# Optimization experiments

Measured on AMD Instinct MI355X. Metric: run time of the kernel, lower is better.

The kernel has to match this reference:

```python
import jax, jax.numpy as jnp
import numpy as np

TOP_K = 2
NUM_EXPERTS = 8
NORM_TOPK_PROB = True


def setup_inputs() -> dict:
    key = jax.random.key(0)
    k0, k1, k2, k3, k4 = jax.random.split(key, 5)
    B, S, H, I, E = 2, 512, 1024, 768, NUM_EXPERTS
    scale = 0.02
    return {
        "hidden_states": jax.random.normal(k0, (B, S, H), dtype=jnp.float32),
        "gate_w": jax.random.normal(k1, (H, E), dtype=jnp.float32) * scale,
        "w_gate": jax.random.normal(k2, (E, H, I), dtype=jnp.float32) * scale,
        "w_up": jax.random.normal(k3, (E, H, I), dtype=jnp.float32) * scale,
        "w_down": jax.random.normal(k4, (E, I, H), dtype=jnp.float32) * scale,
    }


def reference(hidden_states, gate_w, w_gate, w_up, w_down):
    orig_shape = hidden_states.shape
    H = orig_shape[-1]
    x = hidden_states.reshape(-1, H)  # [T, H]
    E = gate_w.shape[-1]

    # Router: softmax in float32, then top-k and optional renormalization.
    router_logits = x @ gate_w  # [T, E]
    routing_probs = jax.nn.softmax(router_logits.astype(jnp.float32), axis=-1)
    routing_weights, selected_experts = jax.lax.top_k(routing_probs, TOP_K)  # [T, K]
    if NORM_TOPK_PROB:
        routing_weights = routing_weights / routing_weights.sum(axis=-1, keepdims=True)
    routing_weights = routing_weights.astype(x.dtype)

    # Combine weights per (token, expert): sum over top-k slots (handles duplicates
    # exactly like the original index_add over per-slot contributions).
    cw = (jax.nn.one_hot(selected_experts, E, dtype=x.dtype)
          * routing_weights[..., None]).sum(axis=1)  # [T, E]

    # Dense per-expert MLP; zero combine weight => zero contribution, matching the
    # gather-MLP-scatter loop's math.
    g = jnp.einsum('th,ehi->tei', x, w_gate)   # [T, E, I]
    u = jnp.einsum('th,ehi->tei', x, w_up)     # [T, E, I]
    a = jax.nn.silu(g) * u                     # [T, E, I]
    y = jnp.einsum('tei,eih->teh', a, w_down)  # [T, E, H]
    out = jnp.einsum('te,teh->th', cw, y)      # [T, H]
    return out.reshape(orig_shape)
```

## Files before the change

### kernel.cpp

```cpp
#include <hip/hip_runtime.h>
#include <hip/hip_bf16.h>

#define HDIM 1024
#define IDIM 768
#define NE   8

typedef __attribute__((ext_vector_type(8))) __bf16 bf16x8;
typedef __attribute__((ext_vector_type(4))) __bf16 bf16x4;
typedef __attribute__((ext_vector_type(4))) float  f32x4;

__device__ __forceinline__ void gload16(const void* g, void* l) {
    __builtin_amdgcn_global_load_lds(
        (const __attribute__((address_space(1))) void*)g,
        (__attribute__((address_space(3))) void*)l, 16, 0, 0);
}

__device__ __forceinline__ int swzoff(int r, int j, int fc) {
    return r * 64 + ((((j << 2) + fc) ^ (r & 7)) << 3);
}

__global__ __launch_bounds__(256) void router_kernel(
    const float* __restrict__ x, const float* __restrict__ gate_w,
    int* __restrict__ counts, int* __restrict__ tok_list,
    int* __restrict__ sel_e, int* __restrict__ sel_pos, float* __restrict__ sel_w,
    int T)
{
    int wave = (blockIdx.x * blockDim.x + threadIdx.x) >> 6;
    int lane = threadIdx.x & 63;
    if (wave >= T) return;
    const float* xr = x + (size_t)wave * HDIM;

    float acc[NE];
    #pragma unroll
    for (int e = 0; e < NE; ++e) acc[e] = 0.f;

    for (int h = lane; h < HDIM; h += 64) {
        float xv = xr[h];
        const float* g = gate_w + (size_t)h * NE;
        #pragma unroll
        for (int e = 0; e < NE; ++e) acc[e] += xv * g[e];
    }
    #pragma unroll
    for (int e = 0; e < NE; ++e) {
        float v = acc[e];
        #pragma unroll
        for (int s = 32; s > 0; s >>= 1) v += __shfl_xor(v, s);
        acc[e] = v;
    }
    if (lane == 0) {
        int e0 = 0;
        #pragma unroll
        for (int e = 1; e < NE; ++e) if (acc[e] > acc[e0]) e0 = e;
        int e1 = -1;
        #pragma unroll
        for (int e = 0; e < NE; ++e) {
            if (e == e0) continue;
            if (e1 < 0 || acc[e] > acc[e1]) e1 = e;
        }
        float d  = __expf(acc[e1] - acc[e0]);
        float w0 = 1.f / (1.f + d);
        float w1 = 1.f - w0;
        int p0 = atomicAdd(&counts[e0], 1);
        tok_list[e0 * T + p0] = wave;
        int p1 = atomicAdd(&counts[e1], 1);
        tok_list[e1 * T + p1] = wave;
        sel_e[wave * 2 + 0] = e0;  sel_pos[wave * 2 + 0] = p0;  sel_w[wave * 2 + 0] = w0;
        sel_e[wave * 2 + 1] = e1;  sel_pos[wave * 2 + 1] = p1;  sel_w[wave * 2 + 1] = w1;
    }
}

__global__ void prefix_kernel(const int* __restrict__ counts, int* __restrict__ offsets)
{
    if (threadIdx.x == 0 && blockIdx.x == 0) {
        int s = 0;
        for (int e = 0; e < NE; ++e) { offsets[e] = s; s += counts[e]; }
    }
}

__global__ __launch_bounds__(256) void gather_x_kernel(
    const float* __restrict__ x, const int* __restrict__ offsets,
    const int* __restrict__ tok_list, __bf16* __restrict__ xg, int T)
{
    int s = (blockIdx.x * blockDim.x + threadIdx.x) >> 6;
    int lane = threadIdx.x & 63;
    if (s >= 2 * T) return;
    int e = 0;
    #pragma unroll
    for (int k = 1; k < NE; ++k) if (s >= offsets[k]) e = k;
    int pos = s - offsets[e];
    int tok = tok_list[e * T + pos];
    const float* xr = x + (size_t)tok * HDIM;
    __bf16* dr = xg + (size_t)s * HDIM;
    for (int j = lane * 4; j < HDIM; j += 256) {
        float4 v = *(const float4*)&xr[j];
        bf16x4 b;
        b[0] = (__bf16)v.x; b[1] = (__bf16)v.y; b[2] = (__bf16)v.z; b[3] = (__bf16)v.w;
        *(bf16x4*)&dr[j] = b;
    }
}

__global__ __launch_bounds__(256) void transpose3_kernel(
    const float* __restrict__ wg, const float* __restrict__ wu, const float* __restrict__ wd,
    __bf16* __restrict__ WgT, __bf16* __restrict__ WuT, __bf16* __restrict__ WdT)
{
    int z = blockIdx.z;
    int mat = z >> 3, e = z & 7;
    const float* src; __bf16* dst; int R, C;
    if (mat == 0)      { src = wg; dst = WgT; R = HDIM; C = IDIM; }
    else if (mat == 1) { src = wu; dst = WuT; R = HDIM; C = IDIM; }
    else               { src = wd; dst = WdT; R = IDIM; C = HDIM; }
    int c0 = blockIdx.x * 64, r0 = blockIdx.y * 64;
    if (c0 >= C || r0 >= R) return;
    src += (size_t)e * R * C;
    dst += (size_t)e * R * C;

    __shared__ __bf16 Lt[64][72];
    int t = threadIdx.x;
    int rin = t >> 4, c4 = (t & 15) * 4;
    #pragma unroll
    for (int rr = 0; rr < 4; ++rr) {
        int r = rr * 16 + rin;
        float4 v = *(const float4*)&src[(size_t)(r0 + r) * C + c0 + c4];
        Lt[c4 + 0][r] = (__bf16)v.x; Lt[c4 + 1][r] = (__bf16)v.y;
        Lt[c4 + 2][r] = (__bf16)v.z; Lt[c4 + 3][r] = (__bf16)v.w;
    }
    __syncthreads();
    int c = t >> 4, r4 = (t & 15) * 4;
    #pragma unroll
    for (int j = 0; j < 4; ++j) {
        int cc = c + j * 16;
        bf16x4 v = *(bf16x4*)&Lt[cc][r4];
        *(bf16x4*)&dst[(size_t)(c0 + cc) * R + r0 + r4] = v;
    }
}

__global__ __launch_bounds__(256) void gateup_mfma_kernel(
    const __bf16* __restrict__ xg,
    const __bf16* __restrict__ WgT, const __bf16* __restrict__ WuT,
    const int* __restrict__ counts, const int* __restrict__ offsets,
    __bf16* __restrict__ Abuf, int T, int nx)
{
    int bid = blockIdx.x;
    int e = bid & 7;
    int rem = bid >> 3;
    int x_t = rem % nx, i_t = rem / nx;
    int n = counts[e];
    int t0 = x_t * 64;
    if (t0 >= n) return;
    int i0 = i_t * 64;
    int base = offsets[e];

    __shared__ __bf16 lds[3 * 3 * 4096];

    int tid = threadIdx.x;
    int w = tid >> 6, lane = tid & 63;
    int wr = w >> 1, wc = w & 1;

    const __bf16* gW = WgT + (size_t)e * IDIM * HDIM;
    const __bf16* uW = WuT + (size_t)e * IDIM * HDIM;
    const __bf16* xS = xg + (size_t)(base + t0) * HDIM;

    int sr0 = w * 16 + (lane >> 3);
    int sr1 = sr0 + 8;
    int sc0 = ((lane & 7) ^ (sr0 & 7)) * 8;
    int sc1 = ((lane & 7) ^ (sr1 & 7)) * 8;
    const __bf16* gp0 = gW + (size_t)(i0 + sr0) * HDIM + sc0;
    const __bf16* gp1 = gW + (size_t)(i0 + sr1) * HDIM + sc1;
    const __bf16* up0 = uW + (size_t)(i0 + sr0) * HDIM + sc0;
    const __bf16* up1 = uW + (size_t)(i0 + sr1) * HDIM + sc1;
    const __bf16* xp0 = xS + (size_t)sr0 * HDIM + sc0;
    const __bf16* xp1 = xS + (size_t)sr1 * HDIM + sc1;
    int dbase = w * 1024;

#define STAGE_GU(buf, kt) { \
    int k0 = (kt) * 64; \
    __bf16* L = lds + (buf) * 12288; \
    gload16(gp0 + k0, L + dbase);                  \
    gload16(gp1 + k0, L + dbase + 512);            \
    gload16(up0 + k0, L + 4096 + dbase);           \
    gload16(up1 + k0, L + 4096 + dbase + 512);     \
    gload16(xp0 + k0, L + 8192 + dbase);           \
    gload16(xp1 + k0, L + 8192 + dbase + 512);     \
}

    f32x4 accg[2][2], accu[2][2];
    #pragma unroll
    for (int a = 0; a < 2; ++a)
        #pragma unroll
        for (int b = 0; b < 2; ++b) { accg[a][b] = (f32x4)0.f; accu[a][b] = (f32x4)0.f; }

    int fr = lane & 15, fc = lane >> 4;
    int ra0 = wc * 32 + fr,  ra1 = ra0 + 16;
    int rb0 = wr * 32 + fr,  rb1 = rb0 + 16;
    int oA0[2] = { swzoff(ra0, 0, fc), swzoff(ra0, 1, fc) };
    int oA1[2] = { swzoff(ra1, 0, fc), swzoff(ra1, 1, fc) };
    int oB0[2] = { swzoff(rb0, 0, fc), swzoff(rb0, 1, fc) };
    int oB1[2] = { swzoff(rb1, 0, fc), swzoff(rb1, 1, fc) };

    const int NK = HDIM / 64;
    STAGE_GU(0, 0);
    STAGE_GU(1, 1);

    for (int kt = 0; kt < NK; ++kt) {
        if (kt < NK - 1) asm volatile("s_waitcnt vmcnt(6)" ::: "memory");
        else             asm volatile("s_waitcnt vmcnt(0)" ::: "memory");
        __builtin_amdgcn_s_barrier();
        if (kt + 2 < NK) STAGE_GU((kt + 2) % 3, kt + 2);
        const __bf16* L  = lds + (kt % 3) * 12288;
        const __bf16* Lg = L;
        const __bf16* Lu = L + 4096;
        const __bf16* Lx = L + 8192;
        #pragma unroll
        for (int j = 0; j < 2; ++j) {
            bf16x8 ag0 = *(const bf16x8*)(Lg + oA0[j]);
            bf16x8 ag1 = *(const bf16x8*)(Lg + oA1[j]);
            bf16x8 au0 = *(const bf16x8*)(Lu + oA0[j]);
            bf16x8 au1 = *(const bf16x8*)(Lu + oA1[j]);
            bf16x8 bx0 = *(const bf16x8*)(Lx + oB0[j]);
            bf16x8 bx1 = *(const bf16x8*)(Lx + oB1[j]);
            accg[0][0] = __builtin_amdgcn_mfma_f32_16x16x32_bf16(ag0, bx0, accg[0][0], 0, 0, 0);
            accg[0][1] = __builtin_amdgcn_mfma_f32_16x16x32_bf16(ag1, bx0, accg[0][1], 0, 0, 0);
            accg[1][0] = __builtin_amdgcn_mfma_f32_16x16x32_bf16(ag0, bx1, accg[1][0], 0, 0, 0);
            accg[1][1] = __builtin_amdgcn_mfma_f32_16x16x32_bf16(ag1, bx1, accg[1][1], 0, 0, 0);
            accu[0][0] = __builtin_amdgcn_mfma_f32_16x16x32_bf16(au0, bx0, accu[0][0], 0, 0, 0);
            accu[0][1] = __builtin_amdgcn_mfma_f32_16x16x32_bf16(au1, bx0, accu[0][1], 0, 0, 0);
            accu[1][0] = __builtin_amdgcn_mfma_f32_16x16x32_bf16(au0, bx1, accu[1][0], 0, 0, 0);
            accu[1][1] = __builtin_amdgcn_mfma_f32_16x16x32_bf16(au1, bx1, accu[1][1], 0, 0, 0);
        }
    }
#undef STAGE_GU

    int dr4 = (lane >> 4) * 4;
    #pragma unroll
    for (int ti = 0; ti < 2; ++ti) {
        int tl = wr * 32 + ti * 16 + fr;
        if (t0 + tl < n) {
            size_t slotrow = (size_t)(base + t0 + tl) * IDIM;
            #pragma unroll
            for (int ii = 0; ii < 2; ++ii) {
                f32x4 g = accg[ti][ii], u = accu[ti][ii];
                bf16x4 o;
                #pragma unroll
                for (int r = 0; r < 4; ++r) {
                    float gv = g[r];
                    float s = gv / (1.f + __expf(-gv));
                    o[r] = (__bf16)(s * u[r]);
                }
                *(bf16x4*)&Abuf[slotrow + i0 + wc * 32 + ii * 16 + dr4] = o;
            }
        }
    }
}

__global__ __launch_bounds__(256) void down_mfma_kernel(
    const __bf16* __restrict__ Abuf, const __bf16* __restrict__ WdT,
    const int* __restrict__ counts, const int* __restrict__ offsets,
    float* __restrict__ Y, int T, int nx)
{
    int bid = blockIdx.x;
    int e = bid & 7;
    int rem = bid >> 3;
    int x_t = rem % nx, h_t = rem / nx;
    int n = counts[e];
    int t0 = x_t * 64;
    if (t0 >= n) return;
    int h0 = h_t * 64;
    int base = offsets[e];

    __shared__ __bf16 lds[3 * 2 * 4096];

    int tid = threadIdx.x;
    int w = tid >> 6, lane = tid & 63;
    int wr = w >> 1, wc = w & 1;

    const __bf16* dW = WdT + (size_t)e * HDIM * IDIM;
    const __bf16* aS = Abuf + (size_t)(base + t0) * IDIM;

    int sr0 = w * 16 + (lane >> 3);
    int sr1 = sr0 + 8;
    int sc0 = ((lane & 7) ^ (sr0 & 7)) * 8;
    int sc1 = ((lane & 7) ^ (sr1 & 7)) * 8;
    const __bf16* wp0 = dW + (size_t)(h0 + sr0) * IDIM + sc0;
    const __bf16* wp1 = dW + (size_t)(h0 + sr1) * IDIM + sc1;
    const __bf16* ap0 = aS + (size_t)sr0 * IDIM + sc0;
    const __bf16* ap1 = aS + (size_t)sr1 * IDIM + sc1;
    int dbase = w * 1024;

#define STAGE_D(buf, kt) { \
    int k0 = (kt) * 64; \
    __bf16* L = lds + (buf) * 8192; \
    gload16(wp0 + k0, L + dbase);              \
    gload16(wp1 + k0, L + dbase + 512);        \
    gload16(ap0 + k0, L + 4096 + dbase);       \
    gload16(ap1 + k0, L + 4096 + dbase + 512); \
}

    f32x4 acc[2][2];
    #pragma unroll
    for (int a = 0; a < 2; ++a)
        #pragma unroll
        for (int b = 0; b < 2; ++b) acc[a][b] = (f32x4)0.f;

    int fr = lane & 15, fc = lane >> 4;
    int ra0 = wc * 32 + fr,  ra1 = ra0 + 16;
    int rb0 = wr * 32 + fr,  rb1 = rb0 + 16;
    int oA0[2] = { swzoff(ra0, 0, fc), swzoff(ra0, 1, fc) };
    int oA1[2] = { swzoff(ra1, 0, fc), swzoff(ra1, 1, fc) };
    int oB0[2] = { swzoff(rb0, 0, fc), swzoff(rb0, 1, fc) };
    int oB1[2] = { swzoff(rb1, 0, fc), swzoff(rb1, 1, fc) };

    const int NK = IDIM / 64;
    STAGE_D(0, 0);
    STAGE_D(1, 1);

    for (int kt = 0; kt < NK; ++kt) {
        if (kt < NK - 1) asm volatile("s_waitcnt vmcnt(4)" ::: "memory");
        else             asm volatile("s_waitcnt vmcnt(0)" ::: "memory");
        __builtin_amdgcn_s_barrier();
        if (kt + 2 < NK) STAGE_D((kt + 2) % 3, kt + 2);
        const __bf16* L  = lds + (kt % 3) * 8192;
        const __bf16* Lw = L;
        const __bf16* La = L + 4096;
        #pragma unroll
        for (int j = 0; j < 2; ++j) {
            bf16x8 aw0 = *(const bf16x8*)(Lw + oA0[j]);
            bf16x8 aw1 = *(const bf16x8*)(Lw + oA1[j]);
            bf16x8 ab0 = *(const bf16x8*)(La + oB0[j]);
            bf16x8 ab1 = *(const bf16x8*)(La + oB1[j]);
            acc[0][0] = __builtin_amdgcn_mfma_f32_16x16x32_bf16(aw0, ab0, acc[0][0], 0, 0, 0);
            acc[0][1] = __builtin_amdgcn_mfma_f32_16x16x32_bf16(aw1, ab0, acc[0][1], 0, 0, 0);
            acc[1][0] = __builtin_amdgcn_mfma_f32_16x16x32_bf16(aw0, ab1, acc[1][0], 0, 0, 0);
            acc[1][1] = __builtin_amdgcn_mfma_f32_16x16x32_bf16(aw1, ab1, acc[1][1], 0, 0, 0);
        }
    }
#undef STAGE_D

    int dr4 = (lane >> 4) * 4;
    #pragma unroll
    for (int si = 0; si < 2; ++si) {
        int sl = wr * 32 + si * 16 + fr;
        if (t0 + sl < n) {
            float* yrow = Y + (size_t)(base + t0 + sl) * HDIM + h0;
            #pragma unroll
            for (int hi = 0; hi < 2; ++hi) {
                f32x4 a = acc[si][hi];
                *(f32x4*)&yrow[wc * 32 + hi * 16 + dr4] = a;
            }
        }
    }
}

__global__ __launch_bounds__(256) void combine_kernel(
    const float* __restrict__ Y, const int* __restrict__ offsets,
    const int* __restrict__ sel_e, const int* __restrict__ sel_pos,
    const float* __restrict__ sel_w, float* __restrict__ out)
{
    int t = blockIdx.x;
    int h4 = threadIdx.x * 4;
    int s0 = offsets[sel_e[t * 2 + 0]] + sel_pos[t * 2 + 0];
    int s1 = offsets[sel_e[t * 2 + 1]] + sel_pos[t * 2 + 1];
    float w0 = sel_w[t * 2 + 0], w1 = sel_w[t * 2 + 1];
    float4 a = *(const float4*)&Y[(size_t)s0 * HDIM + h4];
    float4 b = *(const float4*)&Y[(size_t)s1 * HDIM + h4];
    float4 o;
    o.x = w0 * a.x + w1 * b.x;  o.y = w0 * a.y + w1 * b.y;
    o.z = w0 * a.z + w1 * b.z;  o.w = w0 * a.w + w1 * b.w;
    *(float4*)&out[(size_t)t * HDIM + h4] = o;
}

extern "C" void kernel_launch(void* const* d_in, const int* in_sizes, int n_in,
                              void* d_out, int out_size, void* d_ws, size_t ws_size,
                              hipStream_t stream)
{
    const float* x      = (const float*)d_in[0];
    const float* gate_w = (const float*)d_in[1];
    const float* w_gate = (const float*)d_in[2];
    const float* w_up   = (const float*)d_in[3];
    const float* w_down = (const float*)d_in[4];
    float* out = (float*)d_out;

    int T = in_sizes[0] / HDIM;
    int nx = (T + 63) / 64;

    char* ws = (char*)d_ws;
    size_t o = 0;
    int* counts  = (int*)(ws + o); o += 32;
    int* offsets = (int*)(ws + o); o += 32;
    int* tok_list = (int*)(ws + o); o += (size_t)NE * T * 4;
    o = (o + 255) & ~(size_t)255;
    int*   sel_e   = (int*)(ws + o); o += (size_t)2 * T * 4;
    int*   sel_pos = (int*)(ws + o); o += (size_t)2 * T * 4;
    float* sel_w   = (float*)(ws + o); o += (size_t)2 * T * 4;
    o = (o + 255) & ~(size_t)255;
    __bf16* xg = (__bf16*)(ws + o);   o += (size_t)(2 * T + 64) * HDIM * 2;
    o = (o + 255) & ~(size_t)255;
    __bf16* Abuf = (__bf16*)(ws + o); o += (size_t)(2 * T + 64) * IDIM * 2;
    o = (o + 255) & ~(size_t)255;
    float* Y = (float*)(ws + o);      o += (size_t)(2 * T + 64) * HDIM * 4;
    o = (o + 255) & ~(size_t)255;
    __bf16* WgT = (__bf16*)(ws + o);  o += (size_t)NE * IDIM * HDIM * 2;
    __bf16* WuT = (__bf16*)(ws + o);  o += (size_t)NE * IDIM * HDIM * 2;
    __bf16* WdT = (__bf16*)(ws + o);  o += (size_t)NE * HDIM * IDIM * 2;

    hipMemsetAsync(counts, 0, 32, stream);

    router_kernel<<<(T + 3) / 4, 256, 0, stream>>>(x, gate_w, counts, tok_list,
                                                   sel_e, sel_pos, sel_w, T);
    prefix_kernel<<<1, 64, 0, stream>>>(counts, offsets);
    gather_x_kernel<<<(2 * T + 3) / 4, 256, 0, stream>>>(x, offsets, tok_list, xg, T);

    transpose3_kernel<<<dim3(16, 16, 24), 256, 0, stream>>>(w_gate, w_up, w_down,
                                                            WgT, WuT, WdT);

    gateup_mfma_kernel<<<nx * (IDIM / 64) * NE, 256, 0, stream>>>(
        xg, WgT, WuT, counts, offsets, Abuf, T, nx);

    down_mfma_kernel<<<nx * (HDIM / 64) * NE, 256, 0, stream>>>(
        Abuf, WdT, counts, offsets, Y, T, nx);

    combine_kernel<<<T, 256, 0, stream>>>(Y, offsets, sel_e, sel_pos, sel_w, out);
}
```

Baseline: 193.7 us.

## Fuse weight transpose and bf16 cast into MoE GEMM tile loads

Drops the separate transpose3 kernel that converted all expert weights to transposed bf16 each call. The gate/up and down GEMM kernels now read fp32 weights directly through registers, convert to bf16 and write the tile into swizzled LDS, with a one-stage register prefetch and adjusted waitcnt values. This removes a full read-and-write pass over all weights, but weight tiles are now reloaded in fp32 by every token tile. That doubles bytes per GEMM load and adds conversion work inside the main loop. It also raises wave priority around the MFMA section.

```diff
diff --git a/kernel.cpp b/kernel.cpp
--- a/kernel.cpp
+++ b/kernel.cpp
@@ -99,44 +99,9 @@
     }
 }
 
-__global__ __launch_bounds__(256) void transpose3_kernel(
-    const float* __restrict__ wg, const float* __restrict__ wu, const float* __restrict__ wd,
-    __bf16* __restrict__ WgT, __bf16* __restrict__ WuT, __bf16* __restrict__ WdT)
-{
-    int z = blockIdx.z;
-    int mat = z >> 3, e = z & 7;
-    const float* src; __bf16* dst; int R, C;
-    if (mat == 0)      { src = wg; dst = WgT; R = HDIM; C = IDIM; }
-    else if (mat == 1) { src = wu; dst = WuT; R = HDIM; C = IDIM; }
-    else               { src = wd; dst = WdT; R = IDIM; C = HDIM; }
-    int c0 = blockIdx.x * 64, r0 = blockIdx.y * 64;
-    if (c0 >= C || r0 >= R) return;
-    src += (size_t)e * R * C;
-    dst += (size_t)e * R * C;
-
-    __shared__ __bf16 Lt[64][72];
-    int t = threadIdx.x;
-    int rin = t >> 4, c4 = (t & 15) * 4;
-    #pragma unroll
-    for (int rr = 0; rr < 4; ++rr) {
-        int r = rr * 16 + rin;
-        float4 v = *(const float4*)&src[(size_t)(r0 + r) * C + c0 + c4];
-        Lt[c4 + 0][r] = (__bf16)v.x; Lt[c4 + 1][r] = (__bf16)v.y;
-        Lt[c4 + 2][r] = (__bf16)v.z; Lt[c4 + 3][r] = (__bf16)v.w;
-    }
-    __syncthreads();
-    int c = t >> 4, r4 = (t & 15) * 4;
-    #pragma unroll
-    for (int j = 0; j < 4; ++j) {
-        int cc = c + j * 16;
-        bf16x4 v = *(bf16x4*)&Lt[cc][r4];
-        *(bf16x4*)&dst[(size_t)(c0 + cc) * R + r0 + r4] = v;
-    }
-}
-
 __global__ __launch_bounds__(256) void gateup_mfma_kernel(
     const __bf16* __restrict__ xg,
-    const __bf16* __restrict__ WgT, const __bf16* __restrict__ WuT,
+    const float* __restrict__ w_gate, const float* __restrict__ w_up,
     const int* __restrict__ counts, const int* __restrict__ offsets,
     __bf16* __restrict__ Abuf, int T, int nx)
 {
@@ -150,37 +115,65 @@
     int i0 = i_t * 64;
     int base = offsets[e];
 
-    __shared__ __bf16 lds[3 * 3 * 4096];
+    __shared__ __bf16 lds[3 * 12288];
 
     int tid = threadIdx.x;
     int w = tid >> 6, lane = tid & 63;
     int wr = w >> 1, wc = w & 1;
 
-    const __bf16* gW = WgT + (size_t)e * IDIM * HDIM;
-    const __bf16* uW = WuT + (size_t)e * IDIM * HDIM;
+    const float* gWf = w_gate + (size_t)e * HDIM * IDIM;
+    const float* uWf = w_up   + (size_t)e * HDIM * IDIM;
     const __bf16* xS = xg + (size_t)(base + t0) * HDIM;
 
     int sr0 = w * 16 + (lane >> 3);
     int sr1 = sr0 + 8;
     int sc0 = ((lane & 7) ^ (sr0 & 7)) * 8;
     int sc1 = ((lane & 7) ^ (sr1 & 7)) * 8;
-    const __bf16* gp0 = gW + (size_t)(i0 + sr0) * HDIM + sc0;
-    const __bf16* gp1 = gW + (size_t)(i0 + sr1) * HDIM + sc1;
-    const __bf16* up0 = uW + (size_t)(i0 + sr0) * HDIM + sc0;
-    const __bf16* up1 = uW + (size_t)(i0 + sr1) * HDIM + sc1;
     const __bf16* xp0 = xS + (size_t)sr0 * HDIM + sc0;
     const __bf16* xp1 = xS + (size_t)sr1 * HDIM + sc1;
     int dbase = w * 1024;
 
-#define STAGE_GU(buf, kt) { \
+    const float* gcol = gWf + i0 + lane;
+    const float* ucol = uWf + i0 + lane;
+    int wofs[4];
+    #pragma unroll
+    for (int j = 0; j < 4; ++j) {
+        int h0 = (w + j * 4) * 4;
+        wofs[j] = lane * 64 + ((((h0 >> 3) ^ (lane & 7)) << 3) | (h0 & 7));
+    }
+
+    float rg[4][4], ru[4][4];
+
+#define WLOAD_GU(kt) { \
+    int k0 = (kt) * 64; \
+    _Pragma("unroll") \
+    for (int j = 0; j < 4; ++j) { \
+        int h0 = (w + j * 4) * 4; \
+        const float* gp = gcol + (size_t)(k0 + h0) * IDIM; \
+        const float* up = ucol + (size_t)(k0 + h0) * IDIM; \
+        _Pragma("unroll") \
+        for (int d = 0; d < 4; ++d) { \
+            rg[j][d] = gp[(size_t)d * IDIM]; \
+            ru[j][d] = up[(size_t)d * IDIM]; \
+        } \
+    } \
+}
+#define WWRITE_GU(buf) { \
+    __bf16* L = lds + (buf) * 12288; \
+    _Pragma("unroll") \
+    for (int j = 0; j < 4; ++j) { \
+        bf16x4 gb, ub; \
+        _Pragma("unroll") \
+        for (int d = 0; d < 4; ++d) { gb[d] = (__bf16)rg[j][d]; ub[d] = (__bf16)ru[j][d]; } \
+        *(bf16x4*)&L[wofs[j]] = gb; \
+        *(bf16x4*)&L[4096 + wofs[j]] = ub; \
+    } \
+}
+#define XLOAD_GU(buf, kt) { \
     int k0 = (kt) * 64; \
     __bf16* L = lds + (buf) * 12288; \
-    gload16(gp0 + k0, L + dbase);                  \
-    gload16(gp1 + k0, L + dbase + 512);            \
-    gload16(up0 + k0, L + 4096 + dbase);           \
-    gload16(up1 + k0, L + 4096 + dbase + 512);     \
-    gload16(xp0 + k0, L + 8192 + dbase);           \
-    gload16(xp1 + k0, L + 8192 + dbase + 512);     \
+    gload16(xp0 + k0, L + 8192 + dbase); \
+    gload16(xp1 + k0, L + 8192 + dbase + 512); \
 }
 
     f32x4 accg[2][2], accu[2][2];
@@ -198,18 +191,24 @@
     int oB1[2] = { swzoff(rb1, 0, fc), swzoff(rb1, 1, fc) };
 
     const int NK = HDIM / 64;
-    STAGE_GU(0, 0);
-    STAGE_GU(1, 1);
+    WLOAD_GU(0);
+    XLOAD_GU(0, 0);
+    WWRITE_GU(0);
+    WLOAD_GU(1);
+    XLOAD_GU(1, 1);
 
     for (int kt = 0; kt < NK; ++kt) {
-        if (kt < NK - 1) asm volatile("s_waitcnt vmcnt(6)" ::: "memory");
-        else             asm volatile("s_waitcnt vmcnt(0)" ::: "memory");
+        if (kt < NK - 1) asm volatile("s_waitcnt vmcnt(34) lgkmcnt(0)" ::: "memory");
+        else             asm volatile("s_waitcnt vmcnt(0) lgkmcnt(0)" ::: "memory");
         __builtin_amdgcn_s_barrier();
-        if (kt + 2 < NK) STAGE_GU((kt + 2) % 3, kt + 2);
+        if (kt + 1 < NK) WWRITE_GU((kt + 1) % 3);
+        if (kt + 2 < NK) { WLOAD_GU(kt + 2); XLOAD_GU((kt + 2) % 3, kt + 2); }
+
         const __bf16* L  = lds + (kt % 3) * 12288;
         const __bf16* Lg = L;
         const __bf16* Lu = L + 4096;
         const __bf16* Lx = L + 8192;
+        __builtin_amdgcn_s_setprio(1);
         #pragma unroll
         for (int j = 0; j < 2; ++j) {
             bf16x8 ag0 = *(const bf16x8*)(Lg + oA0[j]);
@@ -227,8 +226,11 @@
             accu[1][0] = __builtin_amdgcn_mfma_f32_16x16x32_bf16(au0, bx1, accu[1][0], 0, 0, 0);
             accu[1][1] = __builtin_amdgcn_mfma_f32_16x16x32_bf16(au1, bx1, accu[1][1], 0, 0, 0);
         }
-    }
-#undef STAGE_GU
+        __builtin_amdgcn_s_setprio(0);
+    }
+#undef WLOAD_GU
+#undef WWRITE_GU
+#undef XLOAD_GU
 
     int dr4 = (lane >> 4) * 4;
     #pragma unroll
@@ -253,7 +255,7 @@
 }
 
 __global__ __launch_bounds__(256) void down_mfma_kernel(
-    const __bf16* __restrict__ Abuf, const __bf16* __restrict__ WdT,
+    const __bf16* __restrict__ Abuf, const float* __restrict__ w_down,
     const int* __restrict__ counts, const int* __restrict__ offsets,
     float* __restrict__ Y, int T, int nx)
 {
@@ -264,34 +266,60 @@
     int n = counts[e];
     int t0 = x_t * 64;
     if (t0 >= n) return;
-    int h0 = h_t * 64;
+    int hb = h_t * 64;
     int base = offsets[e];
 
-    __shared__ __bf16 lds[3 * 2 * 4096];
+    __shared__ __bf16 lds[3 * 8192];
 
     int tid = threadIdx.x;
     int w = tid >> 6, lane = tid & 63;
     int wr = w >> 1, wc = w & 1;
 
-    const __bf16* dW = WdT + (size_t)e * HDIM * IDIM;
+    const float* wdf = w_down + (size_t)e * IDIM * HDIM;
     const __bf16* aS = Abuf + (size_t)(base + t0) * IDIM;
 
     int sr0 = w * 16 + (lane >> 3);
     int sr1 = sr0 + 8;
     int sc0 = ((lane & 7) ^ (sr0 & 7)) * 8;
     int sc1 = ((lane & 7) ^ (sr1 & 7)) * 8;
-    const __bf16* wp0 = dW + (size_t)(h0 + sr0) * IDIM + sc0;
-    const __bf16* wp1 = dW + (size_t)(h0 + sr1) * IDIM + sc1;
     const __bf16* ap0 = aS + (size_t)sr0 * IDIM + sc0;
     const __bf16* ap1 = aS + (size_t)sr1 * IDIM + sc1;
     int dbase = w * 1024;
 
-#define STAGE_D(buf, kt) { \
+    const float* wcol = wdf + hb + lane;
+    int wofs[4];
+    #pragma unroll
+    for (int j = 0; j < 4; ++j) {
+        int ic = (w + j * 4) * 4;
+        wofs[j] = lane * 64 + ((((ic >> 3) ^ (lane & 7)) << 3) | (ic & 7));
+    }
+
+    float rw[4][4];
+
+#define WLOAD_D(kt) { \
+    int k0 = (kt) * 64; \
+    _Pragma("unroll") \
+    for (int j = 0; j < 4; ++j) { \
+        int ic = (w + j * 4) * 4; \
+        const float* wp = wcol + (size_t)(k0 + ic) * HDIM; \
+        _Pragma("unroll") \
+        for (int d = 0; d < 4; ++d) rw[j][d] = wp[(size_t)d * HDIM]; \
+    } \
+}
+#define WWRITE_D(buf) { \
+    __bf16* L = lds + (buf) * 8192; \
+    _Pragma("unroll") \
+    for (int j = 0; j < 4; ++j) { \
+        bf16x4 wb; \
+        _Pragma("unroll") \
+        for (int d = 0; d < 4; ++d) wb[d] = (__bf16)rw[j][d]; \
+        *(bf16x4*)&L[wofs[j]] = wb; \
+    } \
+}
+#define ALOAD_D(buf, kt) { \
     int k0 = (kt) * 64; \
     __bf16* L = lds + (buf) * 8192; \
-    gload16(wp0 + k0, L + dbase);              \
-    gload16(wp1 + k0, L + dbase + 512);        \
-    gload16(ap0 + k0, L + 4096 + dbase);       \
+    gload16(ap0 + k0, L + 4096 + dbase); \
     gload16(ap1 + k0, L + 4096 + dbase + 512); \
 }
 
@@ -310,17 +338,23 @@
     int oB1[2] = { swzoff(rb1, 0, fc), swzoff(rb1, 1, fc) };
 
     const int NK = IDIM / 64;
-    STAGE_D(0, 0);
-    STAGE_D(1, 1);
+    WLOAD_D(0);
+    ALOAD_D(0, 0);
+    WWRITE_D(0);
+    WLOAD_D(1);
+    ALOAD_D(1, 1);
 
     for (int kt = 0; kt < NK; ++kt) {
-        if (kt < NK - 1) asm volatile("s_waitcnt vmcnt(4)" ::: "memory");
-        else             asm volatile("s_waitcnt vmcnt(0)" ::: "memory");
+        if (kt < NK - 1) asm volatile("s_waitcnt vmcnt(18) lgkmcnt(0)" ::: "memory");
+        else             asm volatile("s_waitcnt vmcnt(0) lgkmcnt(0)" ::: "memory");
         __builtin_amdgcn_s_barrier();
-        if (kt + 2 < NK) STAGE_D((kt + 2) % 3, kt + 2);
+        if (kt + 1 < NK) WWRITE_D((kt + 1) % 3);
+        if (kt + 2 < NK) { WLOAD_D(kt + 2); ALOAD_D((kt + 2) % 3, kt + 2); }
+
         const __bf16* L  = lds + (kt % 3) * 8192;
         const __bf16* Lw = L;
         const __bf16* La = L + 4096;
+        __builtin_amdgcn_s_setprio(1);
         #pragma unroll
         for (int j = 0; j < 2; ++j) {
             bf16x8 aw0 = *(const bf16x8*)(Lw + oA0[j]);
@@ -332,15 +366,18 @@
             acc[1][0] = __builtin_amdgcn_mfma_f32_16x16x32_bf16(aw0, ab1, acc[1][0], 0, 0, 0);
             acc[1][1] = __builtin_amdgcn_mfma_f32_16x16x32_bf16(aw1, ab1, acc[1][1], 0, 0, 0);
         }
-    }
-#undef STAGE_D
+        __builtin_amdgcn_s_setprio(0);
+    }
+#undef WLOAD_D
+#undef WWRITE_D
+#undef ALOAD_D
 
     int dr4 = (lane >> 4) * 4;
     #pragma unroll
     for (int si = 0; si < 2; ++si) {
         int sl = wr * 32 + si * 16 + fr;
         if (t0 + sl < n) {
-            float* yrow = Y + (size_t)(base + t0 + sl) * HDIM + h0;
+            float* yrow = Y + (size_t)(base + t0 + sl) * HDIM + hb;
             #pragma unroll
             for (int hi = 0; hi < 2; ++hi) {
                 f32x4 a = acc[si][hi];
@@ -397,10 +434,6 @@
     __bf16* Abuf = (__bf16*)(ws + o); o += (size_t)(2 * T + 64) * IDIM * 2;
     o = (o + 255) & ~(size_t)255;
     float* Y = (float*)(ws + o);      o += (size_t)(2 * T + 64) * HDIM * 4;
-    o = (o + 255) & ~(size_t)255;
-    __bf16* WgT = (__bf16*)(ws + o);  o += (size_t)NE * IDIM * HDIM * 2;
-    __bf16* WuT = (__bf16*)(ws + o);  o += (size_t)NE * IDIM * HDIM * 2;
-    __bf16* WdT = (__bf16*)(ws + o);  o += (size_t)NE * HDIM * IDIM * 2;
 
     hipMemsetAsync(counts, 0, 32, stream);
 
@@ -409,14 +442,11 @@
     prefix_kernel<<<1, 64, 0, stream>>>(counts, offsets);
     gather_x_kernel<<<(2 * T + 3) / 4, 256, 0, stream>>>(x, offsets, tok_list, xg, T);
 
-    transpose3_kernel<<<dim3(16, 16, 24), 256, 0, stream>>>(w_gate, w_up, w_down,
-                                                            WgT, WuT, WdT);
-
     gateup_mfma_kernel<<<nx * (IDIM / 64) * NE, 256, 0, stream>>>(
-        xg, WgT, WuT, counts, offsets, Abuf, T, nx);
+        xg, w_gate, w_up, counts, offsets, Abuf, T, nx);
 
     down_mfma_kernel<<<nx * (HDIM / 64) * NE, 256, 0, stream>>>(
-        Abuf, WdT, counts, offsets, Y, T, nx);
+        Abuf, w_down, counts, offsets, Y, T, nx);
 
     combine_kernel<<<T, 256, 0, stream>>>(Y, offsets, sel_e, sel_pos, sel_w, out);
 }
```

Result: slower. 204.9 us (+5.8%).
